# Performance work log

Hardware: AMD Instinct MI355X
Metric: run time of the kernel (lower is better)

Reference implementation:

```python
import jax, jax.numpy as jnp
import numpy as np

NNZ = 16384
OUT_F = 1024
IN_F = 1024


def setup_inputs() -> dict:
    key = jax.random.key(0)
    k1, k2, k3, k4 = jax.random.split(key, 4)
    x = jax.random.normal(k1, (8, 4096, IN_F), dtype=jnp.float32)
    base_weight = (jax.random.normal(k2, (OUT_F, IN_F), dtype=jnp.float32) * 0.02).astype(jnp.float16)
    ortho_values = (jax.random.normal(k3, (NNZ,), dtype=jnp.float32) * 0.02).astype(jnp.float16)
    # unique flat indices (row * in_features + col), matching load_from_weights
    ortho_indices = jax.random.permutation(k4, OUT_F * IN_F)[:NNZ].astype(jnp.int32)
    alpha = jnp.ones((), dtype=jnp.float32)
    return {"x": x, "base_weight": base_weight, "ortho_values": ortho_values,
            "ortho_indices": ortho_indices, "alpha": alpha}


def reference(x, base_weight, ortho_values, ortho_indices, alpha):
    # Y = X @ W_base^T + alpha * (X @ W_ortho^T)  (torch F.linear convention)
    out_f, in_f = base_weight.shape
    lead = x.shape[:-1]
    xf = x.reshape(-1, in_f)  # [tokens, in]
    base_out = xf @ base_weight.astype(jnp.float32).T  # fp16 weight upcast, as in forward

    rows = ortho_indices // in_f
    cols = ortho_indices % in_f
    ortho_matrix = jnp.zeros((out_f, in_f), dtype=jnp.float32).at[rows, cols].set(
        ortho_values.astype(jnp.float32))
    ortho_out = xf @ ortho_matrix.T

    output = base_out + alpha.astype(jnp.float32) * ortho_out
    return output.reshape(*lead, out_f)
```

## Files before the change

### kernel.cpp

```cpp
#include <hip/hip_runtime.h>

#define IN_F 1024
#define OUT_F 1024
#define NNZ 16384

typedef _Float16 f16;
typedef _Float16 f16x8 __attribute__((ext_vector_type(8)));
typedef float f32x4 __attribute__((ext_vector_type(4)));
typedef unsigned short ushort8 __attribute__((ext_vector_type(8)));

#define AS1 __attribute__((address_space(1)))
#define AS3 __attribute__((address_space(3)))


__device__ __forceinline__ int compute_mode(const unsigned short* __restrict__ w,
                                            float* smax, int* semax) {
  int t = threadIdx.x;
  const float* wf = (const float*)w;
  float m32 = fmaxf(fabsf(wf[t]), fabsf(wf[t + 256]));
  int e8 = 0;
#pragma unroll
  for (int j = 0; j < 8; ++j) {
    unsigned short u = w[t * 8 + j];
    int e = (u >> 7) & 0xFF;
    e8 = e > e8 ? e : e8;
  }
  smax[t] = m32; semax[t] = e8;
  __syncthreads();
  for (int s = 128; s > 0; s >>= 1) {
    if (t < s) {
      smax[t] = fmaxf(smax[t], smax[t + s]);
      semax[t] = semax[t] > semax[t + s] ? semax[t] : semax[t + s];
    }
    __syncthreads();
  }
  int m;
  if (!(smax[0] > 1e-6f)) m = 2;
  else if (semax[0] >= 140) m = 0;
  else m = 1;
  return m;
}

__device__ __forceinline__ float load_w(const void* base, size_t i, int mode) {
  if (mode == 0) return ((const float*)base)[i];
  if (mode == 1) {
    unsigned int u = (unsigned int)((const unsigned short*)base)[i] << 16;
    return __uint_as_float(u);
  }
  return (float)((const f16*)base)[i];
}

__global__ void prep_base(const void* __restrict__ base, f16* __restrict__ Wl) {
  __shared__ float smax[256];
  __shared__ int semax[256];
  int mode = compute_mode((const unsigned short*)base, smax, semax);
  int id = blockIdx.x * 256 + threadIdx.x;
  size_t off = (size_t)id * 8;
  f16x8 h;
  if (mode == 0) {
    const float* b = (const float*)base + off;
    float4 v0 = *reinterpret_cast<const float4*>(b);
    float4 v1 = *reinterpret_cast<const float4*>(b + 4);
    h = (f16x8){(f16)v0.x, (f16)v0.y, (f16)v0.z, (f16)v0.w,
                (f16)v1.x, (f16)v1.y, (f16)v1.z, (f16)v1.w};
  } else if (mode == 1) {
    ushort8 uv = *reinterpret_cast<const ushort8*>((const unsigned short*)base + off);
#pragma unroll
    for (int j = 0; j < 8; ++j)
      h[j] = (f16)__uint_as_float((unsigned int)uv[j] << 16);
  } else {
    h = *reinterpret_cast<const f16x8*>((const f16*)base + off);
  }
  *reinterpret_cast<f16x8*>(Wl + off) = h;
}

__global__ void prep_scatter(const void* __restrict__ base,
                             const void* __restrict__ vals,
                             const int* __restrict__ idx,
                             const float* __restrict__ alpha,
                             f16* __restrict__ Wl) {
  __shared__ float smax[256];
  __shared__ int semax[256];
  int mode = compute_mode((const unsigned short*)base, smax, semax);
  int i = blockIdx.x * 256 + threadIdx.x;
  if (i >= NNZ) return;
  int id = idx[i];
  float v = load_w(base, id, mode) + alpha[0] * load_w(vals, i, mode);
  Wl[id] = (f16)v;
}

__global__ void __launch_bounds__(256) conv_x(const float* __restrict__ X,
                                              f16* __restrict__ Xs, int total) {
  int stride = gridDim.x * 256;
  for (int id = blockIdx.x * 256 + threadIdx.x; id < total; id += stride) {
    size_t off = (size_t)id * 8;
    const float* p = X + off;
    float4 v0 = *reinterpret_cast<const float4*>(p);
    float4 v1 = *reinterpret_cast<const float4*>(p + 4);
    f16x8 h = {(f16)v0.x, (f16)v0.y, (f16)v0.z, (f16)v0.w,
               (f16)v1.x, (f16)v1.y, (f16)v1.z, (f16)v1.w};
    *reinterpret_cast<f16x8*>(Xs + off) = h;
  }
}

#define SB0 __builtin_amdgcn_sched_barrier(0)
#define VMW(N) asm volatile("s_waitcnt vmcnt(" #N ")" ::: "memory")


#define ISSUE_A14(QI, KT1, AP)                                                 \
    __builtin_amdgcn_global_load_lds(                                          \
        (const AS1 void*)(X + rowOffA[QI] + (KT1) * 32 + swzcA),               \
        (AS3 void*)(&sAf[((AP) * 4 + (QI)) * 2048 + t * 4]), 16, 0, 0)

#define ISSUE_B14(QI, KTB1, BP)                                                \
    __builtin_amdgcn_global_load_lds(                                          \
        (const AS1 void*)(Wl + rowOffB[QI] + (KTB1) * 64 + swzc),              \
        (AS3 void*)(&sB[((BP) * 4 + (QI)) * 4096 + t * 8]), 16, 0, 0)

#define DSREAD_A14(AP) do {                                                    \
    _Pragma("unroll")                                                          \
    for (int qq_ = 0; qq_ < 2; ++qq_) {                                        \
      int qa_ = ((AP) * 4 + wm * 2 + qq_) * 2048;                              \
      _Pragma("unroll")                                                        \
      for (int mf_ = 0; mf_ < 4; ++mf_) {                                      \
        int r_ = mf_ * 16 + lr;                                                \
        f32x4 a0_ = *reinterpret_cast<const f32x4*>(                           \
            &sAf[qa_ + r_ * 32 + (((2 * lk) ^ (r_ & 7)) << 2)]);               \
        f32x4 a1_ = *reinterpret_cast<const f32x4*>(                           \
            &sAf[qa_ + r_ * 32 + (((2 * lk + 1) ^ (r_ & 7)) << 2)]);           \
        afr[qq_][mf_] = (f16x8){(f16)a0_[0], (f16)a0_[1], (f16)a0_[2],         \
                                (f16)a0_[3], (f16)a1_[0], (f16)a1_[1],         \
                                (f16)a1_[2], (f16)a1_[3]};                     \
      }                                                                        \
    }                                                                          \
  } while (0)

#define DSREAD_B14(BP, S_) do {                                                \
    int qb_ = ((BP) * 4 + wn) * 4096;                                          \
    _Pragma("unroll")                                                          \
    for (int nf_ = 0; nf_ < 4; ++nf_) {                                        \
      int r_ = nf_ * 16 + lr;                                                  \
      int blk_ = ((S_) * 4 + lk) ^ (lr & 7);                                   \
      bfr[nf_] = *reinterpret_cast<const f16x8*>(&sB[qb_ + r_ * 64 + blk_ * 8]); \
    }                                                                          \
  } while (0)

#define MFMA32_14 do {                                                         \
    __builtin_amdgcn_s_setprio(1);                                             \
    _Pragma("unroll")                                                          \
    for (int qq_ = 0; qq_ < 2; ++qq_)                                          \
      _Pragma("unroll")                                                        \
      for (int mf_ = 0; mf_ < 4; ++mf_)                                        \
        _Pragma("unroll")                                                      \
        for (int nf_ = 0; nf_ < 4; ++nf_)                                      \
          acc[qq_ * 4 + mf_][nf_] = __builtin_amdgcn_mfma_f32_16x16x32_f16(    \
              afr[qq_][mf_], bfr[nf_], acc[qq_ * 4 + mf_][nf_], 0, 0, 0);      \
    __builtin_amdgcn_s_setprio(0);                                             \
  } while (0)

#define KTILE14(AP, BP, S_, KT, ISSB, ISSA, VMN, GATE) do {                    \
    DSREAD_A14(AP);                                                            \
    DSREAD_B14(BP, S_);                                                        \
    if (ISSB) {                                                                \
      ISSUE_B14(0, ((KT) >> 1) + 1, (((KT) >> 1) + 1) & 1);                    \
      ISSUE_B14(1, ((KT) >> 1) + 1, (((KT) >> 1) + 1) & 1);                    \
      ISSUE_B14(2, ((KT) >> 1) + 1, (((KT) >> 1) + 1) & 1);                    \
      ISSUE_B14(3, ((KT) >> 1) + 1, (((KT) >> 1) + 1) & 1); }                  \
    MFMA32_14;                                                                 \
    if (ISSA) {                                                                \
      ISSUE_A14(0, (KT) + 2, ((KT) + 2) % 3);                                  \
      ISSUE_A14(1, (KT) + 2, ((KT) + 2) % 3);                                  \
      ISSUE_A14(2, (KT) + 2, ((KT) + 2) % 3);                                  \
      ISSUE_A14(3, (KT) + 2, ((KT) + 2) % 3); }                                \
    if (GATE) {                                                                \
      VMW(VMN);                                                                \
      __builtin_amdgcn_s_barrier();             \
      SB0;                                                    \
    }                                                                          \
  } while (0)

__global__ void __launch_bounds__(512, 2) gemm14(const float* __restrict__ X,
                                                 const f16* __restrict__ Wl,
                                                 float* __restrict__ C) {
  extern __shared__ char lds[];
  float* sAf = (float*)lds;
  f16* sB = (f16*)(lds + 98304);

  int bidx = blockIdx.x;
  int q = gridDim.x >> 3;
  int wg = (bidx & 7) * q + (bidx >> 3);
  int mt = wg >> 2, nt = wg & 3;

  int t = threadIdx.x;
  int lane = t & 63;
  int w = t >> 6;
  int wm = w >> 2;
  int wn = w & 3;
  int lr = lane & 15;
  int lk = lane >> 4;

  int rS = t >> 3;
  int swzc = (((t & 7) ^ (rS & 7)) << 3);
  int swzcA = (((t & 7) ^ (rS & 7)) << 2);
  size_t rowOffA[4], rowOffB[4];
#pragma unroll
  for (int qi = 0; qi < 4; ++qi) {
    rowOffA[qi] = (size_t)(mt * 256 + qi * 64 + rS) * IN_F;
    rowOffB[qi] = (size_t)(nt * 256 + qi * 64 + rS) * IN_F;
  }

  f16x8 afr[2][4], bfr[4];
  f32x4 acc[8][4];
#pragma unroll
  for (int i = 0; i < 8; ++i)
#pragma unroll
    for (int j = 0; j < 4; ++j)
      acc[i][j] = (f32x4){0.f, 0.f, 0.f, 0.f};

  ISSUE_A14(0, 0, 0); ISSUE_A14(1, 0, 0); ISSUE_A14(2, 0, 0); ISSUE_A14(3, 0, 0);
  ISSUE_B14(0, 0, 0); ISSUE_B14(1, 0, 0); ISSUE_B14(2, 0, 0); ISSUE_B14(3, 0, 0);
  ISSUE_A14(0, 1, 1); ISSUE_A14(1, 1, 1); ISSUE_A14(2, 1, 1); ISSUE_A14(3, 1, 1);
  VMW(4);
  __builtin_amdgcn_s_barrier();
  SB0;

  KTILE14(0, 0, 0,  0, true,  true,  8, true);
  KTILE14(1, 0, 1,  1, false, true,  4, true);
  KTILE14(2, 1, 0,  2, true,  true,  8, true);
  KTILE14(0, 1, 1,  3, false, true,  4, true);
  KTILE14(1, 0, 0,  4, true,  true,  8, true);
  KTILE14(2, 0, 1,  5, false, true,  4, true);
  KTILE14(0, 1, 0,  6, true,  true,  8, true);
  KTILE14(1, 1, 1,  7, false, true,  4, true);
  KTILE14(2, 0, 0,  8, true,  true,  8, true);
  KTILE14(0, 0, 1,  9, false, true,  4, true);
  KTILE14(1, 1, 0, 10, true,  true,  8, true);
  KTILE14(2, 1, 1, 11, false, true,  4, true);
  KTILE14(0, 0, 0, 12, true,  true,  8, true);
  KTILE14(1, 0, 1, 13, false, true,  4, true);
  KTILE14(2, 1, 0, 14, true,  true,  8, true);
  KTILE14(0, 1, 1, 15, false, true,  4, true);
  KTILE14(1, 0, 0, 16, true,  true,  8, true);
  KTILE14(2, 0, 1, 17, false, true,  4, true);
  KTILE14(0, 1, 0, 18, true,  true,  8, true);
  KTILE14(1, 1, 1, 19, false, true,  4, true);
  KTILE14(2, 0, 0, 20, true,  true,  8, true);
  KTILE14(0, 0, 1, 21, false, true,  4, true);
  KTILE14(1, 1, 0, 22, true,  true,  8, true);
  KTILE14(2, 1, 1, 23, false, true,  4, true);
  KTILE14(0, 0, 0, 24, true,  true,  8, true);
  KTILE14(1, 0, 1, 25, false, true,  4, true);
  KTILE14(2, 1, 0, 26, true,  true,  8, true);
  KTILE14(0, 1, 1, 27, false, true,  4, true);
  KTILE14(1, 0, 0, 28, true,  true,  8, true);
  KTILE14(2, 0, 1, 29, false, true,  4, true);
  KTILE14(0, 1, 0, 30, false, false, 0, true);
  KTILE14(1, 1, 1, 31, false, false, 0, false);

  float* Cw = C + (size_t)(mt * 256 + wm * 128 + lk * 4) * OUT_F + nt * 256 + wn * 64 + lr;
#pragma unroll
  for (int m = 0; m < 8; ++m) {
    int rowo = (m >> 2) * 64 + (m & 3) * 16;
#pragma unroll
    for (int nf = 0; nf < 4; ++nf)
#pragma unroll
      for (int g = 0; g < 4; ++g)
        Cw[(size_t)(rowo + g) * OUT_F + nf * 16] = acc[m][nf][g];
  }
}


#define ISSUE_QA11(QI, KT1, AP)                                                \
    __builtin_amdgcn_global_load_lds(                                          \
        (const AS1 void*)(Xs + rowOffA[QI] + (KT1) * 64 + swzc),               \
        (AS3 void*)(&sA[((AP) * 4 + (QI)) * 4096 + t * 8]), 16, 0, 0)

#define ISSUE_QB11(QI, KT1, BP)                                                \
    __builtin_amdgcn_global_load_lds(                                          \
        (const AS1 void*)(Wl + rowOffB[QI] + (KT1) * 64 + swzc),               \
        (AS3 void*)(&sB[((BP) * 4 + (QI)) * 4096 + t * 8]), 16, 0, 0)

#define DSREAD11(AP, BP, S_) do {                                              \
    _Pragma("unroll")                                                          \
    for (int qq_ = 0; qq_ < 2; ++qq_) {                                        \
      int qa_ = ((AP) * 4 + wm * 2 + qq_) * 4096;                              \
      _Pragma("unroll")                                                        \
      for (int mf_ = 0; mf_ < 4; ++mf_) {                                      \
        int r_ = mf_ * 16 + lr;                                                \
        int blk_ = ((S_) * 4 + lk) ^ (lr & 7);                                 \
        afr[qq_][mf_] = *reinterpret_cast<const f16x8*>(&sA[qa_ + r_ * 64 + blk_ * 8]); \
      }                                                                        \
    }                                                                          \
    int qb_ = ((BP) * 4 + wn) * 4096;                                          \
    _Pragma("unroll")                                                          \
    for (int nf_ = 0; nf_ < 4; ++nf_) {                                        \
      int r_ = nf_ * 16 + lr;                                                  \
      int blk_ = ((S_) * 4 + lk) ^ (lr & 7);                                   \
      bfr[nf_] = *reinterpret_cast<const f16x8*>(&sB[qb_ + r_ * 64 + blk_ * 8]); \
    }                                                                          \
  } while (0)

#define KTILE12(AP, BP, KT, ISSB, ISSA, VMN, LASTBAR) do {                     \
    DSREAD11(AP, BP, 0);                                                       \
    if (ISSB) {                                                                \
      ISSUE_QB11(0, (KT) + 1, ((KT) + 1) & 1); ISSUE_QB11(1, (KT) + 1, ((KT) + 1) & 1); \
      ISSUE_QB11(2, (KT) + 1, ((KT) + 1) & 1); ISSUE_QB11(3, (KT) + 1, ((KT) + 1) & 1); } \
    MFMA32_14;                                                                 \
    DSREAD11(AP, BP, 1);                                                       \
    if (ISSA) {                                                                \
      ISSUE_QA11(0, (KT) + 2, ((KT) + 2) % 3); ISSUE_QA11(1, (KT) + 2, ((KT) + 2) % 3); \
      ISSUE_QA11(2, (KT) + 2, ((KT) + 2) % 3); ISSUE_QA11(3, (KT) + 2, ((KT) + 2) % 3); } \
    MFMA32_14;                                                                 \
    if (LASTBAR) {                                                             \
      VMW(VMN);                                                                \
      __builtin_amdgcn_s_barrier();                                            \
      SB0;                                                                     \
    }                                                                          \
  } while (0)

__global__ void __launch_bounds__(512, 2) gemm12(const f16* __restrict__ Xs,
                                                 const f16* __restrict__ Wl,
                                                 float* __restrict__ C) {
  extern __shared__ char lds[];
  f16* sA = (f16*)lds;
  f16* sB = (f16*)(lds + 98304);

  int bidx = blockIdx.x;
  int q = gridDim.x >> 3;
  int wg = (bidx & 7) * q + (bidx >> 3);
  int mt = wg >> 2, nt = wg & 3;

  int t = threadIdx.x;
  int lane = t & 63;
  int w = t >> 6;
  int wm = w >> 2;
  int wn = w & 3;
  int lr = lane & 15;
  int lk = lane >> 4;

  int rS = t >> 3;
  int swzc = (((t & 7) ^ (rS & 7)) << 3);
  size_t rowOffA[4], rowOffB[4];
#pragma unroll
  for (int qi = 0; qi < 4; ++qi) {
    rowOffA[qi] = (size_t)(mt * 256 + qi * 64 + rS) * IN_F;
    rowOffB[qi] = (size_t)(nt * 256 + qi * 64 + rS) * IN_F;
  }

  f16x8 afr[2][4], bfr[4];
  f32x4 acc[8][4];
#pragma unroll
  for (int i = 0; i < 8; ++i)
#pragma unroll
    for (int j = 0; j < 4; ++j)
      acc[i][j] = (f32x4){0.f, 0.f, 0.f, 0.f};

  ISSUE_QA11(0, 0, 0); ISSUE_QA11(1, 0, 0); ISSUE_QA11(2, 0, 0); ISSUE_QA11(3, 0, 0);
  ISSUE_QB11(0, 0, 0); ISSUE_QB11(1, 0, 0); ISSUE_QB11(2, 0, 0); ISSUE_QB11(3, 0, 0);
  ISSUE_QA11(0, 1, 1); ISSUE_QA11(1, 1, 1); ISSUE_QA11(2, 1, 1); ISSUE_QA11(3, 1, 1);
  VMW(4);
  __builtin_amdgcn_s_barrier();
  SB0;

  KTILE12(0, 0,  0, true,  true,  4, true);
  KTILE12(1, 1,  1, true,  true,  4, true);
  KTILE12(2, 0,  2, true,  true,  4, true);
  KTILE12(0, 1,  3, true,  true,  4, true);
  KTILE12(1, 0,  4, true,  true,  4, true);
  KTILE12(2, 1,  5, true,  true,  4, true);
  KTILE12(0, 0,  6, true,  true,  4, true);
  KTILE12(1, 1,  7, true,  true,  4, true);
  KTILE12(2, 0,  8, true,  true,  4, true);
  KTILE12(0, 1,  9, true,  true,  4, true);
  KTILE12(1, 0, 10, true,  true,  4, true);
  KTILE12(2, 1, 11, true,  true,  4, true);
  KTILE12(0, 0, 12, true,  true,  4, true);
  KTILE12(1, 1, 13, true,  true,  4, true);
  KTILE12(2, 0, 14, true,  false, 0, true);
  KTILE12(0, 1, 15, false, false, 0, false);

  float* Cw = C + (size_t)(mt * 256 + wm * 128 + lk * 4) * OUT_F + nt * 256 + wn * 64 + lr;
#pragma unroll
  for (int m = 0; m < 8; ++m) {
    int rowo = (m >> 2) * 64 + (m & 3) * 16;
#pragma unroll
    for (int nf = 0; nf < 4; ++nf)
#pragma unroll
      for (int g = 0; g < 4; ++g)
        Cw[(size_t)(rowo + g) * OUT_F + nf * 16] = acc[m][nf][g];
  }
}

extern "C" void kernel_launch(void* const* d_in, const int* in_sizes, int n_in,
                              void* d_out, int out_size, void* d_ws, size_t ws_size,
                              hipStream_t stream) {
  const float* X = (const float*)d_in[0];
  const void* base = d_in[1];
  const void* vals = d_in[2];
  const int* idx = (const int*)d_in[3];
  const float* alpha = (const float*)d_in[4];
  float* out = (float*)d_out;
  f16* Wl = (f16*)d_ws;
  f16* Xs = (f16*)((char*)d_ws + 2 * 1024 * 1024 + 4096);

  int M = in_sizes[0] / IN_F;
  int total = (M * IN_F) / 8;

  prep_base<<<dim3(512), dim3(256), 0, stream>>>(base, Wl);
  prep_scatter<<<dim3(64), dim3(256), 0, stream>>>(base, vals, idx, alpha, Wl);

  hipError_t e = hipFuncSetAttribute(reinterpret_cast<const void*>(&gemm14),
                                     hipFuncAttributeMaxDynamicSharedMemorySize, 163840);
  if (e == hipSuccess) {
    gemm14<<<dim3((M / 256) * 4), dim3(512), 163840, stream>>>(X, Wl, out);
  } else {
    (void)hipFuncSetAttribute(reinterpret_cast<const void*>(&gemm12),
                              hipFuncAttributeMaxDynamicSharedMemorySize, 163840);
    conv_x<<<dim3(2048), dim3(256), 0, stream>>>(X, Xs, total);
    gemm12<<<dim3((M / 256) * 4), dim3(512), 163840, stream>>>(Xs, Wl, out);
  }
}
```

Before: 104.9 us.

## Load fp32 X through registers and convert to fp16 before LDS store

Adds a gemm15 kernel that loads fp32 activations into registers one k-tile ahead, converts them to fp16, and writes them into a double-buffered fp16 LDS A tile. B still streams directly to LDS with a 3-stage ring. This halves A's LDS footprint and removes the per-fragment fp32-to-fp16 conversion on LDS reads that gemm14 did. In exchange it costs extra VGPRs for the staged registers and a register-to-LDS write on each tile. gemm15 becomes the default path and gemm14 the fallback; the conv_x plus gemm12 path is removed.

```diff
diff --git a/kernel.cpp b/kernel.cpp
--- a/kernel.cpp
+++ b/kernel.cpp
@@ -89,22 +89,164 @@
   Wl[id] = (f16)v;
 }
 
-__global__ void __launch_bounds__(256) conv_x(const float* __restrict__ X,
-                                              f16* __restrict__ Xs, int total) {
-  int stride = gridDim.x * 256;
-  for (int id = blockIdx.x * 256 + threadIdx.x; id < total; id += stride) {
-    size_t off = (size_t)id * 8;
-    const float* p = X + off;
-    float4 v0 = *reinterpret_cast<const float4*>(p);
-    float4 v1 = *reinterpret_cast<const float4*>(p + 4);
-    f16x8 h = {(f16)v0.x, (f16)v0.y, (f16)v0.z, (f16)v0.w,
-               (f16)v1.x, (f16)v1.y, (f16)v1.z, (f16)v1.w};
-    *reinterpret_cast<f16x8*>(Xs + off) = h;
-  }
-}
-
 #define SB0 __builtin_amdgcn_sched_barrier(0)
 #define VMW(N) asm volatile("s_waitcnt vmcnt(" #N ")" ::: "memory")
+#define LGKM0 asm volatile("s_waitcnt lgkmcnt(0)" ::: "memory")
+
+
+#define ISSUE_B15(QI, KT1, BP)                                                 \
+    __builtin_amdgcn_global_load_lds(                                          \
+        (const AS1 void*)(Wl + rowOffB[QI] + (KT1) * 64 + swzc),               \
+        (AS3 void*)(&sB[((BP) * 4 + (QI)) * 4096 + t * 8]), 16, 0, 0)
+
+#define A_LOADS15(KT1) do {                                                    \
+    _Pragma("unroll")                                                          \
+    for (int qi_ = 0; qi_ < 4; ++qi_) {                                        \
+      const float* p_ = X + rowOffA[qi_] + (KT1) * 64 + swzc;                  \
+      ar[2 * qi_]     = *reinterpret_cast<const float4*>(p_);                  \
+      ar[2 * qi_ + 1] = *reinterpret_cast<const float4*>(p_ + 4);              \
+    }                                                                          \
+  } while (0)
+
+#define A_WRITE15(AP1) do {                                                    \
+    _Pragma("unroll")                                                          \
+    for (int qi_ = 0; qi_ < 4; ++qi_) {                                        \
+      float4 v0_ = ar[2 * qi_], v1_ = ar[2 * qi_ + 1];                         \
+      f16x8 h_ = {(f16)v0_.x, (f16)v0_.y, (f16)v0_.z, (f16)v0_.w,              \
+                  (f16)v1_.x, (f16)v1_.y, (f16)v1_.z, (f16)v1_.w};             \
+      *reinterpret_cast<f16x8*>(&sA[((AP1) * 4 + qi_) * 4096 + t * 8]) = h_;   \
+    }                                                                          \
+  } while (0)
+
+#define DSREAD15(AP, BPr, S_) do {                                             \
+    _Pragma("unroll")                                                          \
+    for (int qq_ = 0; qq_ < 2; ++qq_) {                                        \
+      int qa_ = ((AP) * 4 + wm * 2 + qq_) * 4096;                              \
+      _Pragma("unroll")                                                        \
+      for (int mf_ = 0; mf_ < 4; ++mf_) {                                      \
+        int r_ = mf_ * 16 + lr;                                                \
+        int blk_ = ((S_) * 4 + lk) ^ (lr & 7);                                 \
+        afr[qq_][mf_] = *reinterpret_cast<const f16x8*>(&sA[qa_ + r_ * 64 + blk_ * 8]); \
+      }                                                                        \
+    }                                                                          \
+    int qb_ = ((BPr) * 4 + wn) * 4096;                                         \
+    _Pragma("unroll")                                                          \
+    for (int nf_ = 0; nf_ < 4; ++nf_) {                                        \
+      int r_ = nf_ * 16 + lr;                                                  \
+      int blk_ = ((S_) * 4 + lk) ^ (lr & 7);                                   \
+      bfr[nf_] = *reinterpret_cast<const f16x8*>(&sB[qb_ + r_ * 64 + blk_ * 8]); \
+    }                                                                          \
+  } while (0)
+
+#define MFMA32_15 do {                                                         \
+    __builtin_amdgcn_s_setprio(1);                                             \
+    _Pragma("unroll")                                                          \
+    for (int qq_ = 0; qq_ < 2; ++qq_)                                          \
+      _Pragma("unroll")                                                        \
+      for (int mf_ = 0; mf_ < 4; ++mf_)                                        \
+        _Pragma("unroll")                                                      \
+        for (int nf_ = 0; nf_ < 4; ++nf_)                                      \
+          acc[qq_ * 4 + mf_][nf_] = __builtin_amdgcn_mfma_f32_16x16x32_f16(    \
+              afr[qq_][mf_], bfr[nf_], acc[qq_ * 4 + mf_][nf_], 0, 0, 0);      \
+    __builtin_amdgcn_s_setprio(0);                                             \
+  } while (0)
+
+#define KTILE15(AP, BPr, KT, LD_A, ISSB, VMN, GATE) do {                       \
+    if (LD_A) { A_LOADS15((KT) + 1); }                                         \
+    if (ISSB) { ISSUE_B15(0, (KT) + 2, ((KT) + 2) % 3);                        \
+                ISSUE_B15(1, (KT) + 2, ((KT) + 2) % 3);                        \
+                ISSUE_B15(2, (KT) + 2, ((KT) + 2) % 3);                        \
+                ISSUE_B15(3, (KT) + 2, ((KT) + 2) % 3); }                      \
+    SB0;                                                  \
+    DSREAD15(AP, BPr, 0);                                                      \
+    MFMA32_15;                                                                 \
+    DSREAD15(AP, BPr, 1);                                                      \
+    MFMA32_15;                                                                 \
+    if (LD_A) { A_WRITE15((AP) ^ 1); }                   \
+    if (GATE) {                                                                \
+      LGKM0;                                 \
+      VMW(VMN);                                                                \
+      __builtin_amdgcn_s_barrier();             \
+      SB0;                                                    \
+    }                                                                          \
+  } while (0)
+
+__global__ void __launch_bounds__(512, 2) gemm15(const float* __restrict__ X,
+                                                 const f16* __restrict__ Wl,
+                                                 float* __restrict__ C) {
+  extern __shared__ char lds[];
+  f16* sA = (f16*)lds;
+  f16* sB = (f16*)(lds + 65536);
+
+  int bidx = blockIdx.x;
+  int q = gridDim.x >> 3;
+  int wg = (bidx & 7) * q + (bidx >> 3);
+  int mt = wg >> 2, nt = wg & 3;
+
+  int t = threadIdx.x;
+  int lane = t & 63;
+  int w = t >> 6;
+  int wm = w >> 2;
+  int wn = w & 3;
+  int lr = lane & 15;
+  int lk = lane >> 4;
+
+  int rS = t >> 3;
+  int swzc = (((t & 7) ^ (rS & 7)) << 3);
+  size_t rowOffA[4], rowOffB[4];
+#pragma unroll
+  for (int qi = 0; qi < 4; ++qi) {
+    rowOffA[qi] = (size_t)(mt * 256 + qi * 64 + rS) * IN_F;
+    rowOffB[qi] = (size_t)(nt * 256 + qi * 64 + rS) * IN_F;
+  }
+
+  float4 ar[8];
+  f16x8 afr[2][4], bfr[4];
+  f32x4 acc[8][4];
+#pragma unroll
+  for (int i = 0; i < 8; ++i)
+#pragma unroll
+    for (int j = 0; j < 4; ++j)
+      acc[i][j] = (f32x4){0.f, 0.f, 0.f, 0.f};
+
+  A_LOADS15(0);
+  ISSUE_B15(0, 0, 0); ISSUE_B15(1, 0, 0); ISSUE_B15(2, 0, 0); ISSUE_B15(3, 0, 0);
+  ISSUE_B15(0, 1, 1); ISSUE_B15(1, 1, 1); ISSUE_B15(2, 1, 1); ISSUE_B15(3, 1, 1);
+  SB0;
+  A_WRITE15(0);
+  LGKM0;
+  VMW(4);
+  __builtin_amdgcn_s_barrier();
+  SB0;
+
+  KTILE15(0, 0,  0, true,  true,  4, true);
+  KTILE15(1, 1,  1, true,  true,  4, true);
+  KTILE15(0, 2,  2, true,  true,  4, true);
+  KTILE15(1, 0,  3, true,  true,  4, true);
+  KTILE15(0, 1,  4, true,  true,  4, true);
+  KTILE15(1, 2,  5, true,  true,  4, true);
+  KTILE15(0, 0,  6, true,  true,  4, true);
+  KTILE15(1, 1,  7, true,  true,  4, true);
+  KTILE15(0, 2,  8, true,  true,  4, true);
+  KTILE15(1, 0,  9, true,  true,  4, true);
+  KTILE15(0, 1, 10, true,  true,  4, true);
+  KTILE15(1, 2, 11, true,  true,  4, true);
+  KTILE15(0, 0, 12, true,  true,  4, true);
+  KTILE15(1, 1, 13, true,  true,  4, true);
+  KTILE15(0, 2, 14, true,  false, 0, true);
+  KTILE15(1, 0, 15, false, false, 0, false);
+
+  float* Cw = C + (size_t)(mt * 256 + wm * 128 + lk * 4) * OUT_F + nt * 256 + wn * 64 + lr;
+#pragma unroll
+  for (int m = 0; m < 8; ++m) {
+    int rowo = (m >> 2) * 64 + (m & 3) * 16;
+#pragma unroll
+    for (int nf = 0; nf < 4; ++nf)
+#pragma unroll
+      for (int g = 0; g < 4; ++g)
+        Cw[(size_t)(rowo + g) * OUT_F + nf * 16] = acc[m][nf][g];
+  }
+}
 
 
 #define ISSUE_A14(QI, KT1, AP)                                                 \
@@ -145,19 +287,6 @@
     }                                                                          \
   } while (0)
 
-#define MFMA32_14 do {                                                         \
-    __builtin_amdgcn_s_setprio(1);                                             \
-    _Pragma("unroll")                                                          \
-    for (int qq_ = 0; qq_ < 2; ++qq_)                                          \
-      _Pragma("unroll")                                                        \
-      for (int mf_ = 0; mf_ < 4; ++mf_)                                        \
-        _Pragma("unroll")                                                      \
-        for (int nf_ = 0; nf_ < 4; ++nf_)                                      \
-          acc[qq_ * 4 + mf_][nf_] = __builtin_amdgcn_mfma_f32_16x16x32_f16(    \
-              afr[qq_][mf_], bfr[nf_], acc[qq_ * 4 + mf_][nf_], 0, 0, 0);      \
-    __builtin_amdgcn_s_setprio(0);                                             \
-  } while (0)
-
 #define KTILE14(AP, BP, S_, KT, ISSB, ISSA, VMN, GATE) do {                    \
     DSREAD_A14(AP);                                                            \
     DSREAD_B14(BP, S_);                                                        \
@@ -166,7 +295,7 @@
       ISSUE_B14(1, ((KT) >> 1) + 1, (((KT) >> 1) + 1) & 1);                    \
       ISSUE_B14(2, ((KT) >> 1) + 1, (((KT) >> 1) + 1) & 1);                    \
       ISSUE_B14(3, ((KT) >> 1) + 1, (((KT) >> 1) + 1) & 1); }                  \
-    MFMA32_14;                                                                 \
+    MFMA32_15;                                                                 \
     if (ISSA) {                                                                \
       ISSUE_A14(0, (KT) + 2, ((KT) + 2) % 3);                                  \
       ISSUE_A14(1, (KT) + 2, ((KT) + 2) % 3);                                  \
@@ -174,8 +303,8 @@
       ISSUE_A14(3, (KT) + 2, ((KT) + 2) % 3); }                                \
     if (GATE) {                                                                \
       VMW(VMN);                                                                \
-      __builtin_amdgcn_s_barrier();             \
-      SB0;                                                    \
+      __builtin_amdgcn_s_barrier();                                            \
+      SB0;                                                                     \
     }                                                                          \
   } while (0)
 
@@ -269,128 +398,6 @@
   }
 }
 
-
-#define ISSUE_QA11(QI, KT1, AP)                                                \
-    __builtin_amdgcn_global_load_lds(                                          \
-        (const AS1 void*)(Xs + rowOffA[QI] + (KT1) * 64 + swzc),               \
-        (AS3 void*)(&sA[((AP) * 4 + (QI)) * 4096 + t * 8]), 16, 0, 0)
-
-#define ISSUE_QB11(QI, KT1, BP)                                                \
-    __builtin_amdgcn_global_load_lds(                                          \
-        (const AS1 void*)(Wl + rowOffB[QI] + (KT1) * 64 + swzc),               \
-        (AS3 void*)(&sB[((BP) * 4 + (QI)) * 4096 + t * 8]), 16, 0, 0)
-
-#define DSREAD11(AP, BP, S_) do {                                              \
-    _Pragma("unroll")                                                          \
-    for (int qq_ = 0; qq_ < 2; ++qq_) {                                        \
-      int qa_ = ((AP) * 4 + wm * 2 + qq_) * 4096;                              \
-      _Pragma("unroll")                                                        \
-      for (int mf_ = 0; mf_ < 4; ++mf_) {                                      \
-        int r_ = mf_ * 16 + lr;                                                \
-        int blk_ = ((S_) * 4 + lk) ^ (lr & 7);                                 \
-        afr[qq_][mf_] = *reinterpret_cast<const f16x8*>(&sA[qa_ + r_ * 64 + blk_ * 8]); \
-      }                                                                        \
-    }                                                                          \
-    int qb_ = ((BP) * 4 + wn) * 4096;                                          \
-    _Pragma("unroll")                                                          \
-    for (int nf_ = 0; nf_ < 4; ++nf_) {                                        \
-      int r_ = nf_ * 16 + lr;                                                  \
-      int blk_ = ((S_) * 4 + lk) ^ (lr & 7);                                   \
-      bfr[nf_] = *reinterpret_cast<const f16x8*>(&sB[qb_ + r_ * 64 + blk_ * 8]); \
-    }                                                                          \
-  } while (0)
-
-#define KTILE12(AP, BP, KT, ISSB, ISSA, VMN, LASTBAR) do {                     \
-    DSREAD11(AP, BP, 0);                                                       \
-    if (ISSB) {                                                                \
-      ISSUE_QB11(0, (KT) + 1, ((KT) + 1) & 1); ISSUE_QB11(1, (KT) + 1, ((KT) + 1) & 1); \
-      ISSUE_QB11(2, (KT) + 1, ((KT) + 1) & 1); ISSUE_QB11(3, (KT) + 1, ((KT) + 1) & 1); } \
-    MFMA32_14;                                                                 \
-    DSREAD11(AP, BP, 1);                                                       \
-    if (ISSA) {                                                                \
-      ISSUE_QA11(0, (KT) + 2, ((KT) + 2) % 3); ISSUE_QA11(1, (KT) + 2, ((KT) + 2) % 3); \
-      ISSUE_QA11(2, (KT) + 2, ((KT) + 2) % 3); ISSUE_QA11(3, (KT) + 2, ((KT) + 2) % 3); } \
-    MFMA32_14;                                                                 \
-    if (LASTBAR) {                                                             \
-      VMW(VMN);                                                                \
-      __builtin_amdgcn_s_barrier();                                            \
-      SB0;                                                                     \
-    }                                                                          \
-  } while (0)
-
-__global__ void __launch_bounds__(512, 2) gemm12(const f16* __restrict__ Xs,
-                                                 const f16* __restrict__ Wl,
-                                                 float* __restrict__ C) {
-  extern __shared__ char lds[];
-  f16* sA = (f16*)lds;
-  f16* sB = (f16*)(lds + 98304);
-
-  int bidx = blockIdx.x;
-  int q = gridDim.x >> 3;
-  int wg = (bidx & 7) * q + (bidx >> 3);
-  int mt = wg >> 2, nt = wg & 3;
-
-  int t = threadIdx.x;
-  int lane = t & 63;
-  int w = t >> 6;
-  int wm = w >> 2;
-  int wn = w & 3;
-  int lr = lane & 15;
-  int lk = lane >> 4;
-
-  int rS = t >> 3;
-  int swzc = (((t & 7) ^ (rS & 7)) << 3);
-  size_t rowOffA[4], rowOffB[4];
-#pragma unroll
-  for (int qi = 0; qi < 4; ++qi) {
-    rowOffA[qi] = (size_t)(mt * 256 + qi * 64 + rS) * IN_F;
-    rowOffB[qi] = (size_t)(nt * 256 + qi * 64 + rS) * IN_F;
-  }
-
-  f16x8 afr[2][4], bfr[4];
-  f32x4 acc[8][4];
-#pragma unroll
-  for (int i = 0; i < 8; ++i)
-#pragma unroll
-    for (int j = 0; j < 4; ++j)
-      acc[i][j] = (f32x4){0.f, 0.f, 0.f, 0.f};
-
-  ISSUE_QA11(0, 0, 0); ISSUE_QA11(1, 0, 0); ISSUE_QA11(2, 0, 0); ISSUE_QA11(3, 0, 0);
-  ISSUE_QB11(0, 0, 0); ISSUE_QB11(1, 0, 0); ISSUE_QB11(2, 0, 0); ISSUE_QB11(3, 0, 0);
-  ISSUE_QA11(0, 1, 1); ISSUE_QA11(1, 1, 1); ISSUE_QA11(2, 1, 1); ISSUE_QA11(3, 1, 1);
-  VMW(4);
-  __builtin_amdgcn_s_barrier();
-  SB0;
-
-  KTILE12(0, 0,  0, true,  true,  4, true);
-  KTILE12(1, 1,  1, true,  true,  4, true);
-  KTILE12(2, 0,  2, true,  true,  4, true);
-  KTILE12(0, 1,  3, true,  true,  4, true);
-  KTILE12(1, 0,  4, true,  true,  4, true);
-  KTILE12(2, 1,  5, true,  true,  4, true);
-  KTILE12(0, 0,  6, true,  true,  4, true);
-  KTILE12(1, 1,  7, true,  true,  4, true);
-  KTILE12(2, 0,  8, true,  true,  4, true);
-  KTILE12(0, 1,  9, true,  true,  4, true);
-  KTILE12(1, 0, 10, true,  true,  4, true);
-  KTILE12(2, 1, 11, true,  true,  4, true);
-  KTILE12(0, 0, 12, true,  true,  4, true);
-  KTILE12(1, 1, 13, true,  true,  4, true);
-  KTILE12(2, 0, 14, true,  false, 0, true);
-  KTILE12(0, 1, 15, false, false, 0, false);
-
-  float* Cw = C + (size_t)(mt * 256 + wm * 128 + lk * 4) * OUT_F + nt * 256 + wn * 64 + lr;
-#pragma unroll
-  for (int m = 0; m < 8; ++m) {
-    int rowo = (m >> 2) * 64 + (m & 3) * 16;
-#pragma unroll
-    for (int nf = 0; nf < 4; ++nf)
-#pragma unroll
-      for (int g = 0; g < 4; ++g)
-        Cw[(size_t)(rowo + g) * OUT_F + nf * 16] = acc[m][nf][g];
-  }
-}
-
 extern "C" void kernel_launch(void* const* d_in, const int* in_sizes, int n_in,
                               void* d_out, int out_size, void* d_ws, size_t ws_size,
                               hipStream_t stream) {
@@ -401,22 +408,19 @@
   const float* alpha = (const float*)d_in[4];
   float* out = (float*)d_out;
   f16* Wl = (f16*)d_ws;
-  f16* Xs = (f16*)((char*)d_ws + 2 * 1024 * 1024 + 4096);
 
   int M = in_sizes[0] / IN_F;
-  int total = (M * IN_F) / 8;
 
   prep_base<<<dim3(512), dim3(256), 0, stream>>>(base, Wl);
   prep_scatter<<<dim3(64), dim3(256), 0, stream>>>(base, vals, idx, alpha, Wl);
 
-  hipError_t e = hipFuncSetAttribute(reinterpret_cast<const void*>(&gemm14),
+  hipError_t e = hipFuncSetAttribute(reinterpret_cast<const void*>(&gemm15),
                                      hipFuncAttributeMaxDynamicSharedMemorySize, 163840);
   if (e == hipSuccess) {
+    gemm15<<<dim3((M / 256) * 4), dim3(512), 163840, stream>>>(X, Wl, out);
+  } else {
+    (void)hipFuncSetAttribute(reinterpret_cast<const void*>(&gemm14),
+                              hipFuncAttributeMaxDynamicSharedMemorySize, 163840);
     gemm14<<<dim3((M / 256) * 4), dim3(512), 163840, stream>>>(X, Wl, out);
-  } else {
-    (void)hipFuncSetAttribute(reinterpret_cast<const void*>(&gemm12),
-                              hipFuncAttributeMaxDynamicSharedMemorySize, 163840);
-    conv_x<<<dim3(2048), dim3(256), 0, stream>>>(X, Xs, total);
-    gemm12<<<dim3((M / 256) * 4), dim3(512), 163840, stream>>>(Xs, Wl, out);
-  }
-}
+  }
+}
```

Result: slower. 117.6 us (+12.0%).
